# Kernel tuning notes

Hardware: AMD Instinct MI355X
Metric: run time of the kernel (lower is better)

The kernel has to match this reference:

```python
import jax, jax.numpy as jnp
import numpy as np

B, IN, H, D, C, K = 4096, 128, 256, 32, 8, 256
HS = D // 2  # structure_filter hidden (latent_dim > 2)
EPS = 1e-6
MAX_NORM = 0.99


def _gelu(t):
    return jax.nn.gelu(t, approximate=False)  # torch nn.GELU default = exact erf


def _project_to_ball(z):
    norm = jnp.maximum(jnp.linalg.norm(z, axis=-1, keepdims=True), EPS)
    scale = jnp.minimum(MAX_NORM / norm, 1.0)
    return z * scale


def _hyperbolic_distance(xp, yp):
    # Poincare-ball distance: arccosh(1 + 2*|x-y|^2 / ((1-|x|^2)(1-|y|^2)))
    sq = jnp.sum((xp - yp) ** 2, axis=-1)
    xn = jnp.sum(xp * xp, axis=-1)
    yn = jnp.sum(yp * yp, axis=-1)
    denom = jnp.maximum((1.0 - xn) * (1.0 - yn), EPS)
    arg = jnp.maximum(1.0 + 2.0 * sq / denom, 1.0 + EPS)
    return jnp.arccosh(arg)


def setup_inputs() -> dict:
    key = jax.random.key(0)
    ks = jax.random.split(key, 14)
    n = lambda k, shape, s: (jax.random.normal(k, shape, dtype=jnp.float32) * s)
    centers = jax.random.normal(ks[7], (C, D), dtype=jnp.float32)
    centers = centers / jnp.maximum(jnp.linalg.norm(centers, axis=-1, keepdims=True), EPS)
    return {
        "x": jax.random.normal(ks[0], (B, IN), dtype=jnp.float32),
        "W1": n(ks[1], (IN, H), 0.05), "b1": jnp.zeros((H,), jnp.float32),
        "W2": n(ks[2], (H, H), 0.05), "b2": jnp.zeros((H,), jnp.float32),
        "Wv": n(ks[3], (H, D), 0.05), "bv": jnp.zeros((D,), jnp.float32),
        "centers": centers,
        "codebook": n(ks[8], (C, K, D), 0.02),
        "Ws1": n(ks[9], (D, HS), 0.1), "bs1": jnp.zeros((HS,), jnp.float32),
        "Ws2": n(ks[10], (HS, D), 0.1), "bs2": jnp.zeros((D,), jnp.float32),
    }


def reference(x, W1, b1, W2, b2, Wv, bv, centers, codebook, Ws1, bs1, Ws2, bs2):
    sg = jax.lax.stop_gradient
    feats = _gelu(_gelu(x @ W1 + b1) @ W2 + b2)          # [B,H]
    v = feats @ Wv + bv                                   # [B,D]
    scores = (v @ centers.T) / jnp.sqrt(jnp.asarray(D, v.dtype))
    router = jax.nn.softmax(scores, axis=-1)              # [B,C]
    K_chart = jnp.argmax(router, axis=1)                  # [B]
    c_bar = router @ centers                              # [B,D]
    v_local = v - c_bar                                   # [B,D]
    diff = v_local[:, None, None, :] - codebook[None]     # [B,C,K,D]
    dist = jnp.sum(diff * diff, axis=-1)                  # [B,C,K]
    indices = jnp.argmin(dist, axis=-1)                   # [B,C]
    z_q_all = codebook[jnp.arange(C)[None, :], indices]   # [B,C,D]
    v_bc = jnp.broadcast_to(v_local[:, None, :], z_q_all.shape)
    v_proj = _project_to_ball(v_bc)
    w_det = sg(router)
    d_cb = _hyperbolic_distance(z_q_all, sg(v_proj))      # [B,C]
    codebook_loss = jnp.sum(jnp.mean(d_cb ** 2 * w_det, axis=0))
    d_cm = _hyperbolic_distance(sg(z_q_all), v_proj)
    commitment = jnp.sum(jnp.mean(d_cm ** 2 * w_det, axis=0))
    vq_loss = codebook_loss + 0.25 * commitment
    z_q_blended = jnp.sum(z_q_all * router[..., None], axis=1)  # [B,D]
    K_code = jnp.take_along_axis(indices, K_chart[:, None], axis=1)[:, 0]
    delta = v_local[:, None, :] - sg(z_q_all)             # [B,C,D]
    z_n_all = _gelu(delta @ Ws1 + bs1) @ Ws2 + bs2        # [B,C,D]
    z_n = jnp.sum(z_n_all * router[..., None], axis=1)    # [B,D]
    z_tex = (v_local - sg(z_q_blended)) - z_n
    z_q_st = v_local + sg(z_q_blended - v_local)
    z_geo = c_bar + z_q_st + z_n
    return (K_chart, K_code, z_n, z_tex, router, z_geo, vq_loss, indices, z_n_all, c_bar, v_local)
```

## Files before the change

### kernel.cpp

```cpp
#include <hip/hip_runtime.h>
#include <math.h>

#define NB 4096
#define NIN 128
#define NH 256
#define ND 32
#define NC 8
#define NK 256
#define NHS 16

#define OFF_KCHART 0
#define OFF_KCODE  4096
#define OFF_ZN     8192
#define OFF_ZTEX   (OFF_ZN + 4096*32)
#define OFF_ROUTER (OFF_ZTEX + 4096*32)
#define OFF_ZGEO   (OFF_ROUTER + 4096*8)
#define OFF_LOSS   (OFF_ZGEO + 4096*32)
#define OFF_IND    (OFF_LOSS + 1)
#define OFF_ZNALL  (OFF_IND + 4096*8)
#define OFF_CBAR   (OFF_ZNALL + 4096*8*32)
#define OFF_VLOC   (OFF_CBAR + 4096*32)

__device__ __forceinline__ float gelu_exact(float x) {
    return x * (erff(x / 1.41421356237309504f) + 1.0f) * 0.5f;
}

template<int K>
__global__ __launch_bounds__(256)
void gemm_bias_gelu(const float* __restrict__ A, const float* __restrict__ W,
                    const float* __restrict__ bias, float* __restrict__ out) {
    const int N = 256;
    __shared__ float sA[32][68];
    __shared__ float sB[32][68];
    const int t  = threadIdx.x;
    const int n0 = blockIdx.x * 64;
    const int r0 = blockIdx.y * 64;
    const int ty = t >> 4, tx = t & 15;
    const int ar = t >> 3, ak = t & 7;
    const int bk = t >> 4, bc = t & 15;

    float4 bias4 = *(const float4*)(bias + n0 + tx * 4);
    float4 pa0, pa1, pb0, pb1;

    pa0 = *(const float4*)(A + (r0 + ar) * K + ak * 4);
    pa1 = *(const float4*)(A + (r0 + ar + 32) * K + ak * 4);
    pb0 = *(const float4*)(W + bk * N + n0 + bc * 4);
    pb1 = *(const float4*)(W + (bk + 16) * N + n0 + bc * 4);

    float acc[4][4];
    #pragma unroll
    for (int i = 0; i < 4; i++)
        #pragma unroll
        for (int j = 0; j < 4; j++) acc[i][j] = 0.f;

    for (int kk = 0; kk < K; kk += 32) {
        sA[ak*4+0][ar] = pa0.x; sA[ak*4+1][ar] = pa0.y;
        sA[ak*4+2][ar] = pa0.z; sA[ak*4+3][ar] = pa0.w;
        sA[ak*4+0][ar+32] = pa1.x; sA[ak*4+1][ar+32] = pa1.y;
        sA[ak*4+2][ar+32] = pa1.z; sA[ak*4+3][ar+32] = pa1.w;
        *(float4*)(&sB[bk][bc*4])      = pb0;
        *(float4*)(&sB[bk+16][bc*4])   = pb1;
        __syncthreads();
        if (kk + 32 < K) {
            pa0 = *(const float4*)(A + (r0 + ar) * K + kk + 32 + ak * 4);
            pa1 = *(const float4*)(A + (r0 + ar + 32) * K + kk + 32 + ak * 4);
            pb0 = *(const float4*)(W + (kk + 32 + bk) * N + n0 + bc * 4);
            pb1 = *(const float4*)(W + (kk + 32 + bk + 16) * N + n0 + bc * 4);
        }
        #pragma unroll
        for (int k = 0; k < 32; k++) {
            float4 av = *(const float4*)(&sA[k][ty * 4]);
            float4 bv = *(const float4*)(&sB[k][tx * 4]);
            float aa[4] = {av.x, av.y, av.z, av.w};
            float bb[4] = {bv.x, bv.y, bv.z, bv.w};
            #pragma unroll
            for (int i = 0; i < 4; i++)
                #pragma unroll
                for (int j = 0; j < 4; j++)
                    acc[i][j] = fmaf(aa[i], bb[j], acc[i][j]);
        }
        __syncthreads();
    }
    float bb4[4] = {bias4.x, bias4.y, bias4.z, bias4.w};
    #pragma unroll
    for (int i = 0; i < 4; i++) {
        int row = r0 + ty * 4 + i;
        float4 o;
        float* op = (float*)&o;
        #pragma unroll
        for (int j = 0; j < 4; j++) op[j] = gelu_exact(acc[i][j] + bb4[j]);
        *(float4*)(out + row * N + n0 + tx * 4) = o;
    }
}

__global__ __launch_bounds__(256)
void router_kernel(const float* __restrict__ feats, const float* __restrict__ Wv,
                   const float* __restrict__ bv, const float* __restrict__ centers,
                   float* __restrict__ out, float* __restrict__ vloc_ws) {
    __shared__ float sWvT[ND][260];
    __shared__ float sCent[NC * ND];
    __shared__ float sV[16][ND + 1];
    __shared__ float sRout[16][NC];
    const int t = threadIdx.x;
    {
        #pragma unroll
        for (int q = 0; q < 8; q++) {
            int id = t + q * 256;
            int k = id >> 3, c4 = (id & 7) * 4;
            float4 w = ((const float4*)Wv)[id];
            sWvT[c4 + 0][k] = w.x;
            sWvT[c4 + 1][k] = w.y;
            sWvT[c4 + 2][k] = w.z;
            sWvT[c4 + 3][k] = w.w;
        }
        if (t < 64) ((float4*)sCent)[t] = ((const float4*)centers)[t];
    }
    __syncthreads();
    const int r = t >> 4, cp = t & 15;
    const int row = blockIdx.x * 16 + r;
    float a0 = bv[cp], a1 = bv[cp + 16];
    const float4* f4 = (const float4*)(feats + row * NH);
    for (int k4 = 0; k4 < NH / 4; k4++) {
        float4 f = f4[k4];
        float4 w0 = *(const float4*)(&sWvT[cp][k4 * 4]);
        float4 w1 = *(const float4*)(&sWvT[cp + 16][k4 * 4]);
        a0 = fmaf(f.x, w0.x, a0); a1 = fmaf(f.x, w1.x, a1);
        a0 = fmaf(f.y, w0.y, a0); a1 = fmaf(f.y, w1.y, a1);
        a0 = fmaf(f.z, w0.z, a0); a1 = fmaf(f.z, w1.z, a1);
        a0 = fmaf(f.w, w0.w, a0); a1 = fmaf(f.w, w1.w, a1);
    }
    sV[r][cp] = a0; sV[r][cp + 16] = a1;
    __syncthreads();
    if (t < 16) {
        const int rr = t, grow = blockIdx.x * 16 + rr;
        float sc[NC];
        float m = -3.4e38f; int kmax = 0;
        #pragma unroll
        for (int c = 0; c < NC; c++) {
            float acc = 0.f;
            #pragma unroll
            for (int k = 0; k < ND; k++) acc = fmaf(sV[rr][k], sCent[c * ND + k], acc);
            acc = acc / 5.65685424949238f;
            sc[c] = acc;
            if (acc > m) { m = acc; kmax = c; }
        }
        float s = 0.f;
        #pragma unroll
        for (int c = 0; c < NC; c++) { float e = expf(sc[c] - m); sc[c] = e; s += e; }
        float inv = 1.f / s;
        #pragma unroll
        for (int c = 0; c < NC; c++) {
            float rv = sc[c] * inv;
            sRout[rr][c] = rv;
            out[OFF_ROUTER + grow * NC + c] = rv;
        }
        out[OFF_KCHART + grow] = (float)kmax;
    }
    __syncthreads();
    #pragma unroll
    for (int j = 0; j < 2; j++) {
        int col = cp + j * 16;
        float cb = 0.f;
        #pragma unroll
        for (int c = 0; c < NC; c++) cb = fmaf(sRout[r][c], sCent[c * ND + col], cb);
        float vl = sV[r][col] - cb;
        out[OFF_CBAR + row * ND + col] = cb;
        out[OFF_VLOC + row * ND + col] = vl;
        vloc_ws[row * ND + col] = vl;
    }
}

__global__ __launch_bounds__(256)
void vq_chart(const float* __restrict__ codebook, const float* __restrict__ vloc_ws,
              const float* __restrict__ Ws1, const float* __restrict__ bs1,
              const float* __restrict__ Ws2, const float* __restrict__ bs2,
              float* __restrict__ out, float* __restrict__ loss_partial) {
    __shared__ float sCB[NK][36];
    __shared__ float sV[64][36];
    __shared__ float sBest[8][64];
    __shared__ int   sBidx[8][64];
    __shared__ int   sSel[64];
    __shared__ float sRoutv[64];
    __shared__ float sPscale[64];
    __shared__ float sLossArr[64];
    __shared__ float sWs1[ND][17];
    __shared__ float sWs2[NHS][33];
    __shared__ float sbs1[NHS], sbs2v[ND];
    const int t = threadIdx.x;
    const int c = blockIdx.x & 7;
    const int row0 = (blockIdx.x >> 3) * 64;

    {
        const float4* src = (const float4*)(codebook + c * NK * ND);
        #pragma unroll
        for (int q = 0; q < 8; q++) {
            int id = t + q * 256;
            int code = id >> 3, kq = (id & 7) * 4;
            *(float4*)(&sCB[code][kq]) = src[id];
        }
        #pragma unroll
        for (int q = 0; q < 2; q++) {
            int id = t + q * 256;
            int rr = id >> 3, kq = (id & 7) * 4;
            *(float4*)(&sV[rr][kq]) = ((const float4*)(vloc_ws + row0 * ND))[id];
        }
    }
    if (t < 128) {
        float4 w = ((const float4*)Ws1)[t];
        int k = t >> 2, o = (t & 3) * 4;
        sWs1[k][o] = w.x; sWs1[k][o+1] = w.y; sWs1[k][o+2] = w.z; sWs1[k][o+3] = w.w;
    } else {
        int u = t - 128;
        float4 w = ((const float4*)Ws2)[u];
        int k = u >> 3, o = (u & 7) * 4;
        sWs2[k][o] = w.x; sWs2[k][o+1] = w.y; sWs2[k][o+2] = w.z; sWs2[k][o+3] = w.w;
    }
    if (t < NHS) sbs1[t] = bs1[t];
    else if (t < NHS + ND) sbs2v[t - NHS] = bs2[t - NHS];
    if (t < 64) sRoutv[t] = out[OFF_ROUTER + (row0 + t) * NC + c];
    __syncthreads();

    const int r = t & 31, g = t >> 5;
    float vl0[ND], vl1[ND];
    #pragma unroll
    for (int q = 0; q < 8; q++) {
        float4 a = *(const float4*)(&sV[r][q * 4]);
        vl0[q*4] = a.x; vl0[q*4+1] = a.y; vl0[q*4+2] = a.z; vl0[q*4+3] = a.w;
        float4 b = *(const float4*)(&sV[r + 32][q * 4]);
        vl1[q*4] = b.x; vl1[q*4+1] = b.y; vl1[q*4+2] = b.z; vl1[q*4+3] = b.w;
    }
    float best0 = 3.4e38f, best1 = 3.4e38f;
    int bi0 = 0, bi1 = 0;
    for (int j = 0; j < 32; j++) {
        const int code = g * 32 + j;
        float dot0 = 0.f, dot1 = 0.f, en2 = 0.f;
        #pragma unroll
        for (int q = 0; q < 8; q++) {
            float4 e = *(const float4*)(&sCB[code][q * 4]);
            en2  = fmaf(e.x, e.x, en2);
            dot0 = fmaf(vl0[q*4+0], e.x, dot0); dot1 = fmaf(vl1[q*4+0], e.x, dot1);
            en2  = fmaf(e.y, e.y, en2);
            dot0 = fmaf(vl0[q*4+1], e.y, dot0); dot1 = fmaf(vl1[q*4+1], e.y, dot1);
            en2  = fmaf(e.z, e.z, en2);
            dot0 = fmaf(vl0[q*4+2], e.z, dot0); dot1 = fmaf(vl1[q*4+2], e.z, dot1);
            en2  = fmaf(e.w, e.w, en2);
            dot0 = fmaf(vl0[q*4+3], e.w, dot0); dot1 = fmaf(vl1[q*4+3], e.w, dot1);
        }
        float d0 = en2 - 2.f * dot0;
        float d1 = en2 - 2.f * dot1;
        if (d0 < best0) { best0 = d0; bi0 = code; }
        if (d1 < best1) { best1 = d1; bi1 = code; }
    }
    sBest[g][r] = best0;      sBidx[g][r] = bi0;
    sBest[g][r + 32] = best1; sBidx[g][r + 32] = bi1;
    __syncthreads();
    if (t < 64) {
        float bb = sBest[0][t]; int ii = sBidx[0][t];
        #pragma unroll
        for (int gg = 1; gg < 8; gg++) {
            float v = sBest[gg][t];
            if (v < bb) { bb = v; ii = sBidx[gg][t]; }
        }
        sSel[t] = ii;
        out[OFF_IND + (row0 + t) * NC + c] = (float)ii;
        float vn2 = 0.f;
        #pragma unroll
        for (int k = 0; k < ND; k++) { float v = sV[t][k]; vn2 = fmaf(v, v, vn2); }
        float norm = fmaxf(sqrtf(vn2), 1e-6f);
        sPscale[t] = fminf(0.99f / norm, 1.0f);
    }
    __syncthreads();

    const int i = t & 15, r16 = t >> 4;
    const float b1r = sbs1[i];
    const float bo0 = sbs2v[2*i], bo1 = sbs2v[2*i+1];
    #pragma unroll
    for (int pass = 0; pass < 4; pass++) {
        const int lrow = pass * 16 + r16;
        const int grow = row0 + lrow;
        const int sel = sSel[lrow];
        const float rc = sRoutv[lrow];
        const float ps = sPscale[lrow];
        float acc1 = b1r;
        #pragma unroll
        for (int k = 0; k < ND; k++) {
            float dlt = sV[lrow][k] - sCB[sel][k];
            acc1 = fmaf(dlt, sWs1[k][i], acc1);
        }
        float h = gelu_exact(acc1);
        float a0 = bo0, a1 = bo1;
        #pragma unroll
        for (int k = 0; k < NHS; k++) {
            float s1k = __shfl(h, k, 16);
            a0 = fmaf(s1k, sWs2[k][2*i],   a0);
            a1 = fmaf(s1k, sWs2[k][2*i+1], a1);
        }
        out[OFF_ZNALL + (grow * NC + c) * ND + 2*i]     = a0;
        out[OFF_ZNALL + (grow * NC + c) * ND + 2*i + 1] = a1;
        const float e0 = sCB[sel][2*i], e1 = sCB[sel][2*i+1];
        float yp0 = sV[lrow][2*i] * ps, yp1 = sV[lrow][2*i+1] * ps;
        float d0 = e0 - yp0, d1 = e1 - yp1;
        float sq = fmaf(d0, d0, d1 * d1);
        float xn = fmaf(e0, e0, e1 * e1);
        float yn = fmaf(yp0, yp0, yp1 * yp1);
        #pragma unroll
        for (int m = 1; m < 16; m <<= 1) {
            sq += __shfl_xor(sq, m, 16);
            xn += __shfl_xor(xn, m, 16);
            yn += __shfl_xor(yn, m, 16);
        }
        if (i == 0) {
            float denom = fmaxf((1.f - xn) * (1.f - yn), 1e-6f);
            float arg = fmaxf(1.f + 2.f * sq / denom, 1.f + 1e-6f);
            float dd = acoshf(arg);
            sLossArr[lrow] = dd * dd * rc;
        }
    }
    __syncthreads();
    if (t < 64) {
        float v = sLossArr[t];
        #pragma unroll
        for (int off = 32; off > 0; off >>= 1) v += __shfl_down(v, off, 64);
        if (t == 0) loss_partial[blockIdx.x] = v;
    }
}

__global__ __launch_bounds__(256)
void finalize_kernel(const float* __restrict__ codebook, const float* __restrict__ vloc_ws,
                     float* __restrict__ out) {
    const int gid = blockIdx.x * 256 + threadIdx.x;
    const int row = gid >> 4;
    const int cp = gid & 15;
    float rout[NC]; int ind[NC];
    #pragma unroll
    for (int cc = 0; cc < NC; cc++) {
        rout[cc] = out[OFF_ROUTER + row * NC + cc];
        ind[cc]  = (int)out[OFF_IND + row * NC + cc];
    }
    float zn0 = 0.f, zn1 = 0.f, zq0 = 0.f, zq1 = 0.f;
    #pragma unroll
    for (int cc = 0; cc < NC; cc++) {
        const float rcc = rout[cc];
        zn0 = fmaf(out[OFF_ZNALL + (row * NC + cc) * ND + 2*cp],     rcc, zn0);
        zn1 = fmaf(out[OFF_ZNALL + (row * NC + cc) * ND + 2*cp + 1], rcc, zn1);
        const float* e = codebook + (cc * NK + ind[cc]) * ND + 2*cp;
        zq0 = fmaf(e[0], rcc, zq0);
        zq1 = fmaf(e[1], rcc, zq1);
    }
    const float v0 = vloc_ws[row * ND + 2*cp], v1 = vloc_ws[row * ND + 2*cp + 1];
    const float cb0 = out[OFF_CBAR + row * ND + 2*cp];
    const float cb1 = out[OFF_CBAR + row * ND + 2*cp + 1];
    out[OFF_ZN   + row * ND + 2*cp]     = zn0;
    out[OFF_ZN   + row * ND + 2*cp + 1] = zn1;
    out[OFF_ZTEX + row * ND + 2*cp]     = v0 - zq0 - zn0;
    out[OFF_ZTEX + row * ND + 2*cp + 1] = v1 - zq1 - zn1;
    out[OFF_ZGEO + row * ND + 2*cp]     = cb0 + zq0 + zn0;
    out[OFF_ZGEO + row * ND + 2*cp + 1] = cb1 + zq1 + zn1;
    if (cp == 0) {
        int kc = (int)out[OFF_KCHART + row];
        out[OFF_KCODE + row] = out[OFF_IND + row * NC + kc];
    }
}

__global__ __launch_bounds__(256)
void loss_reduce(const float* __restrict__ partials, float* __restrict__ out) {
    int t = threadIdx.x;
    float v = partials[t] + partials[t + 256];
    #pragma unroll
    for (int off = 32; off > 0; off >>= 1) v += __shfl_down(v, off, 64);
    __shared__ float sTmp[4];
    if ((t & 63) == 0) sTmp[t >> 6] = v;
    __syncthreads();
    if (t == 0) out[OFF_LOSS] = 1.25f * (sTmp[0] + sTmp[1] + sTmp[2] + sTmp[3]) / 4096.f;
}

extern "C" void kernel_launch(void* const* d_in, const int* in_sizes, int n_in,
                              void* d_out, int out_size, void* d_ws, size_t ws_size,
                              hipStream_t stream) {
    const float* x        = (const float*)d_in[0];
    const float* W1       = (const float*)d_in[1];
    const float* b1       = (const float*)d_in[2];
    const float* W2       = (const float*)d_in[3];
    const float* b2       = (const float*)d_in[4];
    const float* Wv       = (const float*)d_in[5];
    const float* bv       = (const float*)d_in[6];
    const float* centers  = (const float*)d_in[7];
    const float* codebook = (const float*)d_in[8];
    const float* Ws1      = (const float*)d_in[9];
    const float* bs1      = (const float*)d_in[10];
    const float* Ws2      = (const float*)d_in[11];
    const float* bs2      = (const float*)d_in[12];
    float* out = (float*)d_out;
    float* ws  = (float*)d_ws;

    float* h1       = ws;
    float* feats    = ws + 4096 * 256;
    float* vloc     = ws + 2 * 4096 * 256;
    float* partials = ws + 2 * 4096 * 256 + 4096 * 32;

    gemm_bias_gelu<128><<<dim3(4, 64), dim3(256), 0, stream>>>(x, W1, b1, h1);
    gemm_bias_gelu<256><<<dim3(4, 64), dim3(256), 0, stream>>>(h1, W2, b2, feats);
    router_kernel<<<dim3(256), dim3(256), 0, stream>>>(feats, Wv, bv, centers, out, vloc);
    vq_chart<<<dim3(512), dim3(256), 0, stream>>>(codebook, vloc, Ws1, bs1, Ws2, bs2, out, partials);
    finalize_kernel<<<dim3(256), dim3(256), 0, stream>>>(codebook, vloc, out);
    loss_reduce<<<dim3(1), dim3(256), 0, stream>>>(partials, out);
}
```

Before: 68.60 us.

## Fuse encoder GEMMs and router into one kernel; merge loss reduce into finalize

Replaces the two tiled GEMM+GELU kernels and the router kernel with one encoder kernel. Each block handles 16 rows end to end, keeping h1 and feats in shared memory, so the h1/feats round trips through global memory and two launches go away. The loss reduction moves into block 0 of the finalize kernel, removing another launch. In exchange, each block now streams the full W1 and W2 for only 16 rows, so weight traffic per row rises. With only 256 blocks and large shared memory per block, occupancy and parallelism may be low.

```diff
diff --git a/kernel.cpp b/kernel.cpp
--- a/kernel.cpp
+++ b/kernel.cpp
@@ -25,129 +25,191 @@
     return x * (erff(x / 1.41421356237309504f) + 1.0f) * 0.5f;
 }
 
-template<int K>
-__global__ __launch_bounds__(256)
-void gemm_bias_gelu(const float* __restrict__ A, const float* __restrict__ W,
-                    const float* __restrict__ bias, float* __restrict__ out) {
-    const int N = 256;
-    __shared__ float sA[32][68];
-    __shared__ float sB[32][68];
-    const int t  = threadIdx.x;
-    const int n0 = blockIdx.x * 64;
-    const int r0 = blockIdx.y * 64;
-    const int ty = t >> 4, tx = t & 15;
-    const int ar = t >> 3, ak = t & 7;
-    const int bk = t >> 4, bc = t & 15;
-
-    float4 bias4 = *(const float4*)(bias + n0 + tx * 4);
-    float4 pa0, pa1, pb0, pb1;
-
-    pa0 = *(const float4*)(A + (r0 + ar) * K + ak * 4);
-    pa1 = *(const float4*)(A + (r0 + ar + 32) * K + ak * 4);
-    pb0 = *(const float4*)(W + bk * N + n0 + bc * 4);
-    pb1 = *(const float4*)(W + (bk + 16) * N + n0 + bc * 4);
-
-    float acc[4][4];
-    #pragma unroll
-    for (int i = 0; i < 4; i++)
-        #pragma unroll
-        for (int j = 0; j < 4; j++) acc[i][j] = 0.f;
-
-    for (int kk = 0; kk < K; kk += 32) {
-        sA[ak*4+0][ar] = pa0.x; sA[ak*4+1][ar] = pa0.y;
-        sA[ak*4+2][ar] = pa0.z; sA[ak*4+3][ar] = pa0.w;
-        sA[ak*4+0][ar+32] = pa1.x; sA[ak*4+1][ar+32] = pa1.y;
-        sA[ak*4+2][ar+32] = pa1.z; sA[ak*4+3][ar+32] = pa1.w;
-        *(float4*)(&sB[bk][bc*4])      = pb0;
-        *(float4*)(&sB[bk+16][bc*4])   = pb1;
-        __syncthreads();
-        if (kk + 32 < K) {
-            pa0 = *(const float4*)(A + (r0 + ar) * K + kk + 32 + ak * 4);
-            pa1 = *(const float4*)(A + (r0 + ar + 32) * K + kk + 32 + ak * 4);
-            pb0 = *(const float4*)(W + (kk + 32 + bk) * N + n0 + bc * 4);
-            pb1 = *(const float4*)(W + (kk + 32 + bk + 16) * N + n0 + bc * 4);
+__global__ __launch_bounds__(256, 1)
+void encoder_kernel(const float* __restrict__ x, const float* __restrict__ W1,
+                    const float* __restrict__ b1, const float* __restrict__ W2,
+                    const float* __restrict__ b2, const float* __restrict__ Wv,
+                    const float* __restrict__ bv, const float* __restrict__ centers,
+                    float* __restrict__ out, float* __restrict__ vloc_ws) {
+    __shared__ float sAT[256][18];
+    __shared__ float sW[32][260];
+    __shared__ float sFR[16][260];
+    __shared__ float sVv[16][34];
+    __shared__ float sCent[256];
+    __shared__ float sScore[16][8];
+    __shared__ float sRout[16][8];
+    const int t = threadIdx.x;
+    const int row0 = blockIdx.x * 16;
+    const int rg = t >> 5;
+    const int cg = t & 31;
+
+    #pragma unroll
+    for (int q = 0; q < 2; q++) {
+        int id = q * 256 + t;
+        int row = id >> 5, f = id & 31;
+        float4 a = *(const float4*)(x + (row0 + row) * NIN + f * 4);
+        sAT[f*4+0][row] = a.x; sAT[f*4+1][row] = a.y;
+        sAT[f*4+2][row] = a.z; sAT[f*4+3][row] = a.w;
+    }
+    if (t < 64) ((float4*)sCent)[t] = ((const float4*)centers)[t];
+
+    float4 pw[8];
+    #pragma unroll
+    for (int q = 0; q < 8; q++) {
+        int id = q * 256 + t; int kr = id >> 6, c4 = (id & 63) * 4;
+        pw[q] = *(const float4*)(W1 + kr * NH + c4);
+    }
+    float acc[2][8];
+    #pragma unroll
+    for (int i = 0; i < 2; i++)
+        #pragma unroll
+        for (int j = 0; j < 8; j++) acc[i][j] = 0.f;
+
+    for (int tile = 0; tile < 4; tile++) {
+        __syncthreads();
+        #pragma unroll
+        for (int q = 0; q < 8; q++) {
+            int id = q * 256 + t; int kr = id >> 6, c4 = (id & 63) * 4;
+            *(float4*)(&sW[kr][c4]) = pw[q];
+        }
+        __syncthreads();
+        if (tile < 3) {
+            #pragma unroll
+            for (int q = 0; q < 8; q++) {
+                int id = q * 256 + t; int kr = id >> 6, c4 = (id & 63) * 4;
+                pw[q] = *(const float4*)(W1 + (tile * 32 + 32 + kr) * NH + c4);
+            }
         }
         #pragma unroll
         for (int k = 0; k < 32; k++) {
-            float4 av = *(const float4*)(&sA[k][ty * 4]);
-            float4 bv = *(const float4*)(&sB[k][tx * 4]);
-            float aa[4] = {av.x, av.y, av.z, av.w};
-            float bb[4] = {bv.x, bv.y, bv.z, bv.w};
-            #pragma unroll
-            for (int i = 0; i < 4; i++)
-                #pragma unroll
-                for (int j = 0; j < 4; j++)
-                    acc[i][j] = fmaf(aa[i], bb[j], acc[i][j]);
-        }
-        __syncthreads();
-    }
-    float bb4[4] = {bias4.x, bias4.y, bias4.z, bias4.w};
-    #pragma unroll
-    for (int i = 0; i < 4; i++) {
-        int row = r0 + ty * 4 + i;
-        float4 o;
-        float* op = (float*)&o;
-        #pragma unroll
-        for (int j = 0; j < 4; j++) op[j] = gelu_exact(acc[i][j] + bb4[j]);
-        *(float4*)(out + row * N + n0 + tx * 4) = o;
-    }
-}
-
-__global__ __launch_bounds__(256)
-void router_kernel(const float* __restrict__ feats, const float* __restrict__ Wv,
-                   const float* __restrict__ bv, const float* __restrict__ centers,
-                   float* __restrict__ out, float* __restrict__ vloc_ws) {
-    __shared__ float sWvT[ND][260];
-    __shared__ float sCent[NC * ND];
-    __shared__ float sV[16][ND + 1];
-    __shared__ float sRout[16][NC];
-    const int t = threadIdx.x;
+            float2 a = *(const float2*)(&sAT[tile * 32 + k][rg * 2]);
+            float4 w0 = *(const float4*)(&sW[k][cg * 8]);
+            float4 w1 = *(const float4*)(&sW[k][cg * 8 + 4]);
+            float wv[8] = {w0.x, w0.y, w0.z, w0.w, w1.x, w1.y, w1.z, w1.w};
+            #pragma unroll
+            for (int j = 0; j < 8; j++) {
+                acc[0][j] = fmaf(a.x, wv[j], acc[0][j]);
+                acc[1][j] = fmaf(a.y, wv[j], acc[1][j]);
+            }
+        }
+    }
+
+    #pragma unroll
+    for (int q = 0; q < 8; q++) {
+        int id = q * 256 + t; int kr = id >> 6, c4 = (id & 63) * 4;
+        pw[q] = *(const float4*)(W2 + kr * NH + c4);
+    }
     {
+        float4 bA = *(const float4*)(b1 + cg * 8);
+        float4 bB = *(const float4*)(b1 + cg * 8 + 4);
+        float bb[8] = {bA.x, bA.y, bA.z, bA.w, bB.x, bB.y, bB.z, bB.w};
+        __syncthreads();
+        #pragma unroll
+        for (int i = 0; i < 2; i++)
+            #pragma unroll
+            for (int j = 0; j < 8; j++)
+                sAT[cg * 8 + j][rg * 2 + i] = gelu_exact(acc[i][j] + bb[j]);
+    }
+
+    float acc2[2][8];
+    #pragma unroll
+    for (int i = 0; i < 2; i++)
+        #pragma unroll
+        for (int j = 0; j < 8; j++) acc2[i][j] = 0.f;
+
+    for (int tile = 0; tile < 8; tile++) {
+        __syncthreads();
         #pragma unroll
         for (int q = 0; q < 8; q++) {
-            int id = t + q * 256;
-            int k = id >> 3, c4 = (id & 7) * 4;
-            float4 w = ((const float4*)Wv)[id];
-            sWvT[c4 + 0][k] = w.x;
-            sWvT[c4 + 1][k] = w.y;
-            sWvT[c4 + 2][k] = w.z;
-            sWvT[c4 + 3][k] = w.w;
-        }
-        if (t < 64) ((float4*)sCent)[t] = ((const float4*)centers)[t];
-    }
-    __syncthreads();
-    const int r = t >> 4, cp = t & 15;
-    const int row = blockIdx.x * 16 + r;
-    float a0 = bv[cp], a1 = bv[cp + 16];
-    const float4* f4 = (const float4*)(feats + row * NH);
-    for (int k4 = 0; k4 < NH / 4; k4++) {
-        float4 f = f4[k4];
-        float4 w0 = *(const float4*)(&sWvT[cp][k4 * 4]);
-        float4 w1 = *(const float4*)(&sWvT[cp + 16][k4 * 4]);
-        a0 = fmaf(f.x, w0.x, a0); a1 = fmaf(f.x, w1.x, a1);
-        a0 = fmaf(f.y, w0.y, a0); a1 = fmaf(f.y, w1.y, a1);
-        a0 = fmaf(f.z, w0.z, a0); a1 = fmaf(f.z, w1.z, a1);
-        a0 = fmaf(f.w, w0.w, a0); a1 = fmaf(f.w, w1.w, a1);
-    }
-    sV[r][cp] = a0; sV[r][cp + 16] = a1;
+            int id = q * 256 + t; int kr = id >> 6, c4 = (id & 63) * 4;
+            *(float4*)(&sW[kr][c4]) = pw[q];
+        }
+        __syncthreads();
+        if (tile < 7) {
+            #pragma unroll
+            for (int q = 0; q < 8; q++) {
+                int id = q * 256 + t; int kr = id >> 6, c4 = (id & 63) * 4;
+                pw[q] = *(const float4*)(W2 + (tile * 32 + 32 + kr) * NH + c4);
+            }
+        }
+        #pragma unroll
+        for (int k = 0; k < 32; k++) {
+            float2 a = *(const float2*)(&sAT[tile * 32 + k][rg * 2]);
+            float4 w0 = *(const float4*)(&sW[k][cg * 8]);
+            float4 w1 = *(const float4*)(&sW[k][cg * 8 + 4]);
+            float wv[8] = {w0.x, w0.y, w0.z, w0.w, w1.x, w1.y, w1.z, w1.w};
+            #pragma unroll
+            for (int j = 0; j < 8; j++) {
+                acc2[0][j] = fmaf(a.x, wv[j], acc2[0][j]);
+                acc2[1][j] = fmaf(a.y, wv[j], acc2[1][j]);
+            }
+        }
+    }
+    {
+        float4 bA = *(const float4*)(b2 + cg * 8);
+        float4 bB = *(const float4*)(b2 + cg * 8 + 4);
+        float bb[8] = {bA.x, bA.y, bA.z, bA.w, bB.x, bB.y, bB.z, bB.w};
+        #pragma unroll
+        for (int i = 0; i < 2; i++)
+            #pragma unroll
+            for (int j = 0; j < 8; j++)
+                sFR[rg * 2 + i][cg * 8 + j] = gelu_exact(acc2[i][j] + bb[j]);
+    }
+    __syncthreads();
+    #pragma unroll
+    for (int q = 0; q < 8; q++) {
+        int id = q * 256 + t; int k = id >> 3, c4 = (id & 7) * 4;
+        float4 w = *(const float4*)(Wv + k * ND + c4);
+        sW[c4+0][k] = w.x; sW[c4+1][k] = w.y; sW[c4+2][k] = w.z; sW[c4+3][k] = w.w;
+    }
+    __syncthreads();
+    {
+        const int r = t >> 4, i = t & 15;
+        const int c0 = (i & 7) * 4, kh = i >> 3;
+        float va[4] = {0.f, 0.f, 0.f, 0.f};
+        #pragma unroll
+        for (int k4 = 0; k4 < 32; k4++) {
+            int k = kh * 128 + k4 * 4;
+            float4 fa = *(const float4*)(&sFR[r][k]);
+            #pragma unroll
+            for (int cj = 0; cj < 4; cj++) {
+                float4 w = *(const float4*)(&sW[c0 + cj][k]);
+                va[cj] = fmaf(fa.x, w.x, va[cj]);
+                va[cj] = fmaf(fa.y, w.y, va[cj]);
+                va[cj] = fmaf(fa.z, w.z, va[cj]);
+                va[cj] = fmaf(fa.w, w.w, va[cj]);
+            }
+        }
+        #pragma unroll
+        for (int cj = 0; cj < 4; cj++) va[cj] += __shfl_xor(va[cj], 8, 16);
+        if (kh == 0) {
+            #pragma unroll
+            for (int cj = 0; cj < 4; cj++) sVv[r][c0 + cj] = va[cj] + bv[c0 + cj];
+        }
+    }
+    __syncthreads();
+    if (t < 128) {
+        int r = t >> 3, c = t & 7;
+        float s = 0.f;
+        #pragma unroll
+        for (int k = 0; k < ND; k++) s = fmaf(sVv[r][k], sCent[c * ND + k], s);
+        sScore[r][c] = s / 5.65685424949238f;
+    }
     __syncthreads();
     if (t < 16) {
-        const int rr = t, grow = blockIdx.x * 16 + rr;
+        const int rr = t, grow = row0 + rr;
         float sc[NC];
         float m = -3.4e38f; int kmax = 0;
         #pragma unroll
         for (int c = 0; c < NC; c++) {
-            float acc = 0.f;
-            #pragma unroll
-            for (int k = 0; k < ND; k++) acc = fmaf(sV[rr][k], sCent[c * ND + k], acc);
-            acc = acc / 5.65685424949238f;
-            sc[c] = acc;
-            if (acc > m) { m = acc; kmax = c; }
-        }
-        float s = 0.f;
-        #pragma unroll
-        for (int c = 0; c < NC; c++) { float e = expf(sc[c] - m); sc[c] = e; s += e; }
-        float inv = 1.f / s;
+            float s = sScore[rr][c];
+            sc[c] = s;
+            if (s > m) { m = s; kmax = c; }
+        }
+        float ssum = 0.f;
+        #pragma unroll
+        for (int c = 0; c < NC; c++) { float e = expf(sc[c] - m); sc[c] = e; ssum += e; }
+        float inv = 1.f / ssum;
         #pragma unroll
         for (int c = 0; c < NC; c++) {
             float rv = sc[c] * inv;
@@ -157,16 +219,20 @@
         out[OFF_KCHART + grow] = (float)kmax;
     }
     __syncthreads();
-    #pragma unroll
-    for (int j = 0; j < 2; j++) {
-        int col = cp + j * 16;
-        float cb = 0.f;
-        #pragma unroll
-        for (int c = 0; c < NC; c++) cb = fmaf(sRout[r][c], sCent[c * ND + col], cb);
-        float vl = sV[r][col] - cb;
-        out[OFF_CBAR + row * ND + col] = cb;
-        out[OFF_VLOC + row * ND + col] = vl;
-        vloc_ws[row * ND + col] = vl;
+    {
+        const int r = t >> 4, i = t & 15;
+        const int row = row0 + r;
+        #pragma unroll
+        for (int j = 0; j < 2; j++) {
+            int col = 2 * i + j;
+            float cb = 0.f;
+            #pragma unroll
+            for (int c = 0; c < NC; c++) cb = fmaf(sRout[r][c], sCent[c * ND + col], cb);
+            float vl = sVv[r][col] - cb;
+            out[OFF_CBAR + row * ND + col] = cb;
+            out[OFF_VLOC + row * ND + col] = vl;
+            vloc_ws[row * ND + col] = vl;
+        }
     }
 }
 
@@ -326,8 +392,8 @@
 }
 
 __global__ __launch_bounds__(256)
-void finalize_kernel(const float* __restrict__ codebook, const float* __restrict__ vloc_ws,
-                     float* __restrict__ out) {
+void finalize2_kernel(const float* __restrict__ codebook, const float* __restrict__ vloc_ws,
+                      float* __restrict__ out, const float* __restrict__ partials) {
     const int gid = blockIdx.x * 256 + threadIdx.x;
     const int row = gid >> 4;
     const int cp = gid & 15;
@@ -360,18 +426,16 @@
         int kc = (int)out[OFF_KCHART + row];
         out[OFF_KCODE + row] = out[OFF_IND + row * NC + kc];
     }
-}
-
-__global__ __launch_bounds__(256)
-void loss_reduce(const float* __restrict__ partials, float* __restrict__ out) {
-    int t = threadIdx.x;
-    float v = partials[t] + partials[t + 256];
-    #pragma unroll
-    for (int off = 32; off > 0; off >>= 1) v += __shfl_down(v, off, 64);
-    __shared__ float sTmp[4];
-    if ((t & 63) == 0) sTmp[t >> 6] = v;
-    __syncthreads();
-    if (t == 0) out[OFF_LOSS] = 1.25f * (sTmp[0] + sTmp[1] + sTmp[2] + sTmp[3]) / 4096.f;
+    if (blockIdx.x == 0) {
+        __shared__ float sTmp[4];
+        const int t = threadIdx.x;
+        float v = partials[t] + partials[t + 256];
+        #pragma unroll
+        for (int off = 32; off > 0; off >>= 1) v += __shfl_down(v, off, 64);
+        if ((t & 63) == 0) sTmp[t >> 6] = v;
+        __syncthreads();
+        if (t == 0) out[OFF_LOSS] = 1.25f * (sTmp[0] + sTmp[1] + sTmp[2] + sTmp[3]) / 4096.f;
+    }
 }
 
 extern "C" void kernel_launch(void* const* d_in, const int* in_sizes, int n_in,
@@ -393,15 +457,10 @@
     float* out = (float*)d_out;
     float* ws  = (float*)d_ws;
 
-    float* h1       = ws;
-    float* feats    = ws + 4096 * 256;
-    float* vloc     = ws + 2 * 4096 * 256;
-    float* partials = ws + 2 * 4096 * 256 + 4096 * 32;
-
-    gemm_bias_gelu<128><<<dim3(4, 64), dim3(256), 0, stream>>>(x, W1, b1, h1);
-    gemm_bias_gelu<256><<<dim3(4, 64), dim3(256), 0, stream>>>(h1, W2, b2, feats);
-    router_kernel<<<dim3(256), dim3(256), 0, stream>>>(feats, Wv, bv, centers, out, vloc);
+    float* vloc     = ws;
+    float* partials = ws + 4096 * 32;
+
+    encoder_kernel<<<dim3(256), dim3(256), 0, stream>>>(x, W1, b1, W2, b2, Wv, bv, centers, out, vloc);
     vq_chart<<<dim3(512), dim3(256), 0, stream>>>(codebook, vloc, Ws1, bs1, Ws2, bs2, out, partials);
-    finalize_kernel<<<dim3(256), dim3(256), 0, stream>>>(codebook, vloc, out);
-    loss_reduce<<<dim3(1), dim3(256), 0, stream>>>(partials, out);
+    finalize2_kernel<<<dim3(256), dim3(256), 0, stream>>>(codebook, vloc, out, partials);
 }
```

New measurement: 92.50 us. +34.9%, slower.

## Load GEMM A operand directly from global into registers and fold loss reduce into finalize

Applied to the files above, without the earlier changes.

The MLP GEMM kernel no longer stages the A tile through shared memory. Each thread loads its own four rows from global memory into registers, with a two-step register prefetch. B stays in shared memory, now double-buffered, which removes the second barrier per k-step. The separate single-block loss reduction launch is merged into block 0 of the finalize kernel, saving one kernel launch. In exchange, A reads become redundant across the 16 threads sharing a row and lose the shared-memory reuse, with uncoalesced strided float4 loads.

```diff
diff --git a/kernel.cpp b/kernel.cpp
--- a/kernel.cpp
+++ b/kernel.cpp
@@ -30,22 +30,37 @@
 void gemm_bias_gelu(const float* __restrict__ A, const float* __restrict__ W,
                     const float* __restrict__ bias, float* __restrict__ out) {
     const int N = 256;
-    __shared__ float sA[32][68];
-    __shared__ float sB[32][68];
+    __shared__ float sB[2][32][68];
     const int t  = threadIdx.x;
     const int n0 = blockIdx.x * 64;
     const int r0 = blockIdx.y * 64;
     const int ty = t >> 4, tx = t & 15;
-    const int ar = t >> 3, ak = t & 7;
     const int bk = t >> 4, bc = t & 15;
 
     float4 bias4 = *(const float4*)(bias + n0 + tx * 4);
-    float4 pa0, pa1, pb0, pb1;
-
-    pa0 = *(const float4*)(A + (r0 + ar) * K + ak * 4);
-    pa1 = *(const float4*)(A + (r0 + ar + 32) * K + ak * 4);
-    pb0 = *(const float4*)(W + bk * N + n0 + bc * 4);
-    pb1 = *(const float4*)(W + (bk + 16) * N + n0 + bc * 4);
+
+    float4 pb0 = *(const float4*)(W + bk * N + n0 + bc * 4);
+    float4 pb1 = *(const float4*)(W + (bk + 16) * N + n0 + bc * 4);
+
+    const float* Ab0 = A + (r0 + ty * 4 + 0) * K;
+    const float* Ab1 = A + (r0 + ty * 4 + 1) * K;
+    const float* Ab2 = A + (r0 + ty * 4 + 2) * K;
+    const float* Ab3 = A + (r0 + ty * 4 + 3) * K;
+    float ac[4][4], an[4][4];
+    {
+        float4 c0 = *(const float4*)(Ab0 + 0), c1 = *(const float4*)(Ab1 + 0);
+        float4 c2 = *(const float4*)(Ab2 + 0), c3 = *(const float4*)(Ab3 + 0);
+        ac[0][0]=c0.x; ac[0][1]=c0.y; ac[0][2]=c0.z; ac[0][3]=c0.w;
+        ac[1][0]=c1.x; ac[1][1]=c1.y; ac[1][2]=c1.z; ac[1][3]=c1.w;
+        ac[2][0]=c2.x; ac[2][1]=c2.y; ac[2][2]=c2.z; ac[2][3]=c2.w;
+        ac[3][0]=c3.x; ac[3][1]=c3.y; ac[3][2]=c3.z; ac[3][3]=c3.w;
+        float4 n0v = *(const float4*)(Ab0 + 4), n1v = *(const float4*)(Ab1 + 4);
+        float4 n2v = *(const float4*)(Ab2 + 4), n3v = *(const float4*)(Ab3 + 4);
+        an[0][0]=n0v.x; an[0][1]=n0v.y; an[0][2]=n0v.z; an[0][3]=n0v.w;
+        an[1][0]=n1v.x; an[1][1]=n1v.y; an[1][2]=n1v.z; an[1][3]=n1v.w;
+        an[2][0]=n2v.x; an[2][1]=n2v.y; an[2][2]=n2v.z; an[2][3]=n2v.w;
+        an[3][0]=n3v.x; an[3][1]=n3v.y; an[3][2]=n3v.z; an[3][3]=n3v.w;
+    }
 
     float acc[4][4];
     #pragma unroll
@@ -53,33 +68,46 @@
         #pragma unroll
         for (int j = 0; j < 4; j++) acc[i][j] = 0.f;
 
+    int buf = 0;
     for (int kk = 0; kk < K; kk += 32) {
-        sA[ak*4+0][ar] = pa0.x; sA[ak*4+1][ar] = pa0.y;
-        sA[ak*4+2][ar] = pa0.z; sA[ak*4+3][ar] = pa0.w;
-        sA[ak*4+0][ar+32] = pa1.x; sA[ak*4+1][ar+32] = pa1.y;
-        sA[ak*4+2][ar+32] = pa1.z; sA[ak*4+3][ar+32] = pa1.w;
-        *(float4*)(&sB[bk][bc*4])      = pb0;
-        *(float4*)(&sB[bk+16][bc*4])   = pb1;
+        *(float4*)(&sB[buf][bk][bc*4])    = pb0;
+        *(float4*)(&sB[buf][bk+16][bc*4]) = pb1;
         __syncthreads();
         if (kk + 32 < K) {
-            pa0 = *(const float4*)(A + (r0 + ar) * K + kk + 32 + ak * 4);
-            pa1 = *(const float4*)(A + (r0 + ar + 32) * K + kk + 32 + ak * 4);
             pb0 = *(const float4*)(W + (kk + 32 + bk) * N + n0 + bc * 4);
             pb1 = *(const float4*)(W + (kk + 32 + bk + 16) * N + n0 + bc * 4);
         }
         #pragma unroll
-        for (int k = 0; k < 32; k++) {
-            float4 av = *(const float4*)(&sA[k][ty * 4]);
-            float4 bv = *(const float4*)(&sB[k][tx * 4]);
-            float aa[4] = {av.x, av.y, av.z, av.w};
-            float bb[4] = {bv.x, bv.y, bv.z, bv.w};
+        for (int c = 0; c < 8; c++) {
+            int knext = kk + (c + 2) * 4;
+            if (knext > K - 4) knext = K - 4;
+            float4 p0 = *(const float4*)(Ab0 + knext);
+            float4 p1 = *(const float4*)(Ab1 + knext);
+            float4 p2 = *(const float4*)(Ab2 + knext);
+            float4 p3 = *(const float4*)(Ab3 + knext);
             #pragma unroll
-            for (int i = 0; i < 4; i++)
+            for (int u = 0; u < 4; u++) {
+                float4 bv = *(const float4*)(&sB[buf][c * 4 + u][tx * 4]);
+                float bb[4] = {bv.x, bv.y, bv.z, bv.w};
                 #pragma unroll
-                for (int j = 0; j < 4; j++)
-                    acc[i][j] = fmaf(aa[i], bb[j], acc[i][j]);
-        }
-        __syncthreads();
+                for (int j = 0; j < 4; j++) {
+                    acc[0][j] = fmaf(ac[0][u], bb[j], acc[0][j]);
+                    acc[1][j] = fmaf(ac[1][u], bb[j], acc[1][j]);
+                    acc[2][j] = fmaf(ac[2][u], bb[j], acc[2][j]);
+                    acc[3][j] = fmaf(ac[3][u], bb[j], acc[3][j]);
+                }
+            }
+            #pragma unroll
+            for (int u = 0; u < 4; u++) {
+                ac[0][u] = an[0][u]; ac[1][u] = an[1][u];
+                ac[2][u] = an[2][u]; ac[3][u] = an[3][u];
+            }
+            an[0][0]=p0.x; an[0][1]=p0.y; an[0][2]=p0.z; an[0][3]=p0.w;
+            an[1][0]=p1.x; an[1][1]=p1.y; an[1][2]=p1.z; an[1][3]=p1.w;
+            an[2][0]=p2.x; an[2][1]=p2.y; an[2][2]=p2.z; an[2][3]=p2.w;
+            an[3][0]=p3.x; an[3][1]=p3.y; an[3][2]=p3.z; an[3][3]=p3.w;
+        }
+        buf ^= 1;
     }
     float bb4[4] = {bias4.x, bias4.y, bias4.z, bias4.w};
     #pragma unroll
@@ -326,8 +354,8 @@
 }
 
 __global__ __launch_bounds__(256)
-void finalize_kernel(const float* __restrict__ codebook, const float* __restrict__ vloc_ws,
-                     float* __restrict__ out) {
+void finalize2_kernel(const float* __restrict__ codebook, const float* __restrict__ vloc_ws,
+                      float* __restrict__ out, const float* __restrict__ partials) {
     const int gid = blockIdx.x * 256 + threadIdx.x;
     const int row = gid >> 4;
     const int cp = gid & 15;
@@ -360,18 +388,16 @@
         int kc = (int)out[OFF_KCHART + row];
         out[OFF_KCODE + row] = out[OFF_IND + row * NC + kc];
     }
-}
-
-__global__ __launch_bounds__(256)
-void loss_reduce(const float* __restrict__ partials, float* __restrict__ out) {
-    int t = threadIdx.x;
-    float v = partials[t] + partials[t + 256];
-    #pragma unroll
-    for (int off = 32; off > 0; off >>= 1) v += __shfl_down(v, off, 64);
-    __shared__ float sTmp[4];
-    if ((t & 63) == 0) sTmp[t >> 6] = v;
-    __syncthreads();
-    if (t == 0) out[OFF_LOSS] = 1.25f * (sTmp[0] + sTmp[1] + sTmp[2] + sTmp[3]) / 4096.f;
+    if (blockIdx.x == 0) {
+        __shared__ float sTmp[4];
+        const int t = threadIdx.x;
+        float v = partials[t] + partials[t + 256];
+        #pragma unroll
+        for (int off = 32; off > 0; off >>= 1) v += __shfl_down(v, off, 64);
+        if ((t & 63) == 0) sTmp[t >> 6] = v;
+        __syncthreads();
+        if (t == 0) out[OFF_LOSS] = 1.25f * (sTmp[0] + sTmp[1] + sTmp[2] + sTmp[3]) / 4096.f;
+    }
 }
 
 extern "C" void kernel_launch(void* const* d_in, const int* in_sizes, int n_in,
@@ -402,6 +428,5 @@
     gemm_bias_gelu<256><<<dim3(4, 64), dim3(256), 0, stream>>>(h1, W2, b2, feats);
     router_kernel<<<dim3(256), dim3(256), 0, stream>>>(feats, Wv, bv, centers, out, vloc);
     vq_chart<<<dim3(512), dim3(256), 0, stream>>>(codebook, vloc, Ws1, bs1, Ws2, bs2, out, partials);
-    finalize_kernel<<<dim3(256), dim3(256), 0, stream>>>(codebook, vloc, out);
-    loss_reduce<<<dim3(1), dim3(256), 0, stream>>>(partials, out);
-}
+    finalize2_kernel<<<dim3(256), dim3(256), 0, stream>>>(codebook, vloc, out, partials);
+}
```

New measurement: 69.60 us. About the same (+1.5%).
